# Kernel tuning notes

Hardware: AMD Instinct MI355X
Metric: run time of the kernel (lower is better)

## Reference

```python
import jax, jax.numpy as jnp
import numpy as np

D_IN = 1024
D_OUT = 1024
N_HEADS = 16
HEAD_DIM = D_OUT // N_HEADS


def setup_inputs() -> dict:
    key = jax.random.key(0)
    ks = jax.random.split(key, 5)
    scale = 0.02
    x = jax.random.normal(ks[0], (2, 2048, D_IN), dtype=jnp.float32)
    Wq = jax.random.normal(ks[1], (D_IN, D_OUT), dtype=jnp.float32) * scale
    Wk = jax.random.normal(ks[2], (D_IN, D_OUT), dtype=jnp.float32) * scale
    Wv = jax.random.normal(ks[3], (D_IN, D_OUT), dtype=jnp.float32) * scale
    Wout = jax.random.normal(ks[4], (D_OUT, D_OUT), dtype=jnp.float32) * scale
    return {"x": x, "Wq": Wq, "Wk": Wk, "Wv": Wv, "Wout": Wout}


def reference(x, Wq, Wk, Wv, Wout):
    batch, seq_len, _ = x.shape
    # projections (no bias)
    Q = (x @ Wq).reshape(batch, seq_len, N_HEADS, HEAD_DIM)
    K = (x @ Wk).reshape(batch, seq_len, N_HEADS, HEAD_DIM)
    V = (x @ Wv).reshape(batch, seq_len, N_HEADS, HEAD_DIM)
    # scores: [batch, heads, seq, seq]
    scores = jnp.einsum("bqhd,bkhd->bhqk", Q, K) / jnp.sqrt(
        jnp.asarray(HEAD_DIM, dtype=x.dtype)
    )
    # causal mask: positions k > q masked to -inf
    causal = jnp.tril(jnp.ones((seq_len, seq_len), dtype=bool))
    scores = jnp.where(causal[None, None], scores, -jnp.inf)
    weights = jax.nn.softmax(scores, axis=-1)
    vectors = jnp.einsum("bhqk,bkhd->bqhd", weights, V)
    vectors = vectors.reshape(batch, seq_len, D_OUT)
    return vectors @ Wout
```

## Files before the change

kernel.cpp:

```cpp
#include <hip/hip_runtime.h>
#include <hip/hip_bf16.h>


typedef __attribute__((ext_vector_type(8))) _Float16 vhalf8;
typedef __attribute__((ext_vector_type(4))) _Float16 vhalf4;
typedef __attribute__((ext_vector_type(4))) float vfloat4;

#define D_MODEL 1024
#define SEQ     2048
#define NB      2
#define NH      16
#define HD      64

#define SCALE_K1 0.18033688f

__device__ __forceinline__ void async16(const void* g, void* l) {
  __builtin_amdgcn_global_load_lds(
      (const __attribute__((address_space(1))) unsigned int*)g,
      (__attribute__((address_space(3))) unsigned int*)l, 16, 0, 0);
}

__global__ __launch_bounds__(256) void prep(
    const float* __restrict__ x,
    const float* __restrict__ Wq, const float* __restrict__ Wk,
    const float* __restrict__ Wv, const float* __restrict__ Wo,
    _Float16* __restrict__ Xh, _Float16* __restrict__ Wt_qkv,
    _Float16* __restrict__ Wot) {
  int z = blockIdx.z;
  int t = threadIdx.x;
  if (z == 4) {
    int id = blockIdx.y * 16 + blockIdx.x;
#pragma unroll
    for (int pass = 0; pass < 8; pass++) {
      size_t i = ((size_t)(pass * 256 + id) * 256 + t) * 8;
      float4 a = *(const float4*)&x[i];
      float4 b = *(const float4*)&x[i + 4];
      vhalf8 h;
      h[0] = (_Float16)a.x; h[1] = (_Float16)a.y;
      h[2] = (_Float16)a.z; h[3] = (_Float16)a.w;
      h[4] = (_Float16)b.x; h[5] = (_Float16)b.y;
      h[6] = (_Float16)b.z; h[7] = (_Float16)b.w;
      *(vhalf8*)&Xh[i] = h;
    }
    return;
  }
  __shared__ _Float16 tile[64][65];
  const float* in = (z == 0) ? Wq : (z == 1) ? Wk : (z == 2) ? Wv : Wo;
  _Float16* out = (z < 3) ? (Wt_qkv + (size_t)z * 1024 * 1024) : Wot;
  int c0 = blockIdx.x * 64, r0 = blockIdx.y * 64;
  int tc = t & 63, tr = t >> 6;
#pragma unroll
  for (int p = 0; p < 16; p++) {
    int r = tr + p * 4;
    tile[r][tc] = (_Float16)in[(size_t)(r0 + r) * 1024 + c0 + tc];
  }
  __syncthreads();
#pragma unroll
  for (int p = 0; p < 16; p++) {
    int r = tr + p * 4;
    out[(size_t)(c0 + r) * 1024 + r0 + tc] = tile[tc][r];
  }
}

template <int BN>
__global__ __launch_bounds__(256) void gemm128(
    const _Float16* __restrict__ A, const _Float16* __restrict__ Bt,
    _Float16* __restrict__ Ch, float* __restrict__ Cf,
    _Float16* __restrict__ Vt, int M, int N, int K, int mode) {
  constexpr int ACH = 8;
  constexpr int BCH = BN / 16;
  constexpr int CPW = (ACH + BCH) / 4;
  constexpr int JN = BN / 32;
  __shared__ _Float16 As[128 * 32];
  __shared__ _Float16 Bs[BN * 32];
  int m0 = blockIdx.x * 128, n0 = blockIdx.y * BN;
  int t = threadIdx.x;
  int lane = t & 63, wave = t >> 6;
  int wm = (wave >> 1) * 64, wn = (wave & 1) * (BN / 2);
  int col = lane & 15, quad = lane >> 4;
  int srow = lane >> 2;
  int gcol = (((lane & 3) ^ (srow & 3)) << 3);

  vfloat4 acc[4][JN];
#pragma unroll
  for (int i = 0; i < 4; i++)
#pragma unroll
    for (int j = 0; j < JN; j++) {
      acc[i][j][0] = 0.f; acc[i][j][1] = 0.f;
      acc[i][j][2] = 0.f; acc[i][j][3] = 0.f;
    }

  int xq = (quad ^ (col & 3)) * 8;

  for (int k0 = 0; k0 < K; k0 += 32) {
    __syncthreads();
#pragma unroll
    for (int j = 0; j < CPW; j++) {
      int c = wave * CPW + j;
      if (c < ACH) {
        int row = c * 16 + srow;
        async16(&A[(size_t)(m0 + row) * K + k0 + gcol], &As[c * 512]);
      } else {
        int row = (c - ACH) * 16 + srow;
        async16(&Bt[(size_t)(n0 + row) * K + k0 + gcol], &Bs[(c - ACH) * 512]);
      }
    }
    __syncthreads();

    vhalf8 af[4], bf[JN];
#pragma unroll
    for (int i = 0; i < 4; i++)
      af[i] = *(const vhalf8*)&As[(wm + i * 16 + col) * 32 + xq];
#pragma unroll
    for (int j = 0; j < JN; j++)
      bf[j] = *(const vhalf8*)&Bs[(wn + j * 16 + col) * 32 + xq];
#pragma unroll
    for (int i = 0; i < 4; i++)
#pragma unroll
      for (int j = 0; j < JN; j++)
        acc[i][j] = __builtin_amdgcn_mfma_f32_16x16x32_f16(af[i], bf[j], acc[i][j], 0, 0, 0);
  }

  bool vmode = (mode == 2) && (n0 >= 2048);
#pragma unroll
  for (int i = 0; i < 4; i++)
#pragma unroll
    for (int j = 0; j < JN; j++) {
      if (vmode) {
        int n = n0 + wn + j * 16 + col;
        int nn = n - 2048;
        int hh = nn >> 6, dd = nn & 63;
        int m_base = m0 + wm + i * 16 + quad * 4;
        int bb = m_base >> 11, ss = m_base & 2047;
        vhalf4 pk;
        pk[0] = (_Float16)acc[i][j][0]; pk[1] = (_Float16)acc[i][j][1];
        pk[2] = (_Float16)acc[i][j][2]; pk[3] = (_Float16)acc[i][j][3];
        *(vhalf4*)&Vt[(((size_t)bb * NH + hh) * HD + dd) * SEQ + ss] = pk;
      } else {
#pragma unroll
        for (int r = 0; r < 4; r++) {
          int m = m0 + wm + i * 16 + quad * 4 + r;
          int n = n0 + wn + j * 16 + col;
          if (mode == 1)
            Cf[(size_t)m * N + n] = acc[i][j][r];
          else
            Ch[(size_t)m * N + n] = (_Float16)acc[i][j][r];
        }
      }
    }
}

__global__ __launch_bounds__(256, 2) void attn(
    const _Float16* __restrict__ QKV, const _Float16* __restrict__ Vt,
    _Float16* __restrict__ Vec) {
  int blk = blockIdx.x;
  int pp = blk >> 5;
  int hb = blk & 31;
  int h = hb & 15;
  int b = hb >> 4;

  const _Float16* Qb  = QKV + (size_t)(b * SEQ) * 3072 + h * HD;
  const _Float16* Kb  = QKV + (size_t)(b * SEQ) * 3072 + 1024 + h * HD;
  const _Float16* Vtb = Vt + (size_t)(b * NH + h) * HD * SEQ;

  int t = threadIdx.x;
  int lane = t & 63, wave = t >> 6;
  int sw = wave & 1, hf = wave >> 1;
  int col = lane & 15, quad = lane >> 4;

  __shared__ union {
    _Float16 Ks[2][64][72];
    float    Om[64][65];
  } su;
  __shared__ _Float16 Vs[2][64][72];
  __shared__ _Float16 Ps[4][32][72];
  __shared__ float Lm[64];

  int tl = t & 127;
  int srow = tl >> 2;
  int scol = (tl & 3) * 16;
  int kslotA = ((srow & 3) << 4) + (srow >> 2);
  int kslotB = kslotA + 8;
  int kcol = scol ^ ((srow & 3) << 4);

  int tiles[2] = {31 - pp, pp};

  vhalf8 krA0, krA1, krB0, krB1, vrA0, vrA1, vrB0, vrB1;
  {
    const _Float16* kg = &Kb[(size_t)(hf * 64 + srow) * 3072 + scol];
    krA0 = *(const vhalf8*)kg; krA1 = *(const vhalf8*)(kg + 8);
    kg += (size_t)32 * 3072;
    krB0 = *(const vhalf8*)kg; krB1 = *(const vhalf8*)(kg + 8);
    const _Float16* vg = &Vtb[(size_t)srow * SEQ + hf * 64 + scol];
    vrA0 = *(const vhalf8*)vg; vrA1 = *(const vhalf8*)(vg + 8);
    vg += (size_t)32 * SEQ;
    vrB0 = *(const vhalf8*)vg; vrB1 = *(const vhalf8*)(vg + 8);
  }

#pragma unroll
  for (int phase = 0; phase < 2; phase++) {
    int qt = tiles[phase];
    int q0 = qt * 64;
    int ntk = qt + 1;
    int J = (ntk + 1) >> 1;
    int wq0 = q0 + sw * 32;

    vhalf8 qf0[2], qf1[2];
#pragma unroll
    for (int qs = 0; qs < 2; qs++) {
      const _Float16* qp = &Qb[(size_t)(wq0 + qs * 16 + col) * 3072 + quad * 8];
      qf0[qs] = *(const vhalf8*)qp;
      qf1[qs] = *(const vhalf8*)(qp + 32);
#pragma unroll
      for (int i = 0; i < 8; i++) {
        qf0[qs][i] = qf0[qs][i] * (_Float16)SCALE_K1;
        qf1[qs][i] = qf1[qs][i] * (_Float16)SCALE_K1;
      }
    }

    vfloat4 o[2][4];
#pragma unroll
    for (int qs = 0; qs < 2; qs++)
#pragma unroll
      for (int i = 0; i < 4; i++) {
        o[qs][i][0] = 0.f; o[qs][i][1] = 0.f;
        o[qs][i][2] = 0.f; o[qs][i][3] = 0.f;
      }
    float lsum[2][4] = {{0.f, 0.f, 0.f, 0.f}, {0.f, 0.f, 0.f, 0.f}};

    for (int j = 0; j < J; j++) {
      int ti = 2 * j + hf;
      bool active = (ti < ntk);
      int kb = ti * 64;
      if (active) {
        *(vhalf8*)&su.Ks[hf][kslotA][kcol]     = krA0;
        *(vhalf8*)&su.Ks[hf][kslotA][kcol + 8] = krA1;
        *(vhalf8*)&su.Ks[hf][kslotB][kcol]     = krB0;
        *(vhalf8*)&su.Ks[hf][kslotB][kcol + 8] = krB1;
        *(vhalf8*)&Vs[hf][srow][scol]          = vrA0;
        *(vhalf8*)&Vs[hf][srow][scol + 8]      = vrA1;
        *(vhalf8*)&Vs[hf][srow + 32][scol]     = vrB0;
        *(vhalf8*)&Vs[hf][srow + 32][scol + 8] = vrB1;
      }
      __syncthreads();

      {
        int tnext;
        if (phase == 0)
          tnext = (ti + 2 < ntk) ? (ti + 2) : hf;
        else
          tnext = (ti + 2 < ntk) ? (ti + 2) : ti;
        int kpf = tnext * 64;
        const _Float16* kg = &Kb[(size_t)(kpf + srow) * 3072 + scol];
        krA0 = *(const vhalf8*)kg; krA1 = *(const vhalf8*)(kg + 8);
        kg += (size_t)32 * 3072;
        krB0 = *(const vhalf8*)kg; krB1 = *(const vhalf8*)(kg + 8);
        const _Float16* vg = &Vtb[(size_t)srow * SEQ + kpf + scol];
        vrA0 = *(const vhalf8*)vg; vrA1 = *(const vhalf8*)(vg + 8);
        vg += (size_t)32 * SEQ;
        vrB0 = *(const vhalf8*)vg; vrB1 = *(const vhalf8*)(vg + 8);
      }

      if (active) {
        vhalf8 kf[4][2];
#pragma unroll
        for (int hh = 0; hh < 4; hh++) {
          int swz = hh << 4;
          kf[hh][0] = *(const vhalf8*)&su.Ks[hf][hh * 16 + col][(quad * 8) ^ swz];
          kf[hh][1] = *(const vhalf8*)&su.Ks[hf][hh * 16 + col][(32 + quad * 8) ^ swz];
        }
#pragma unroll
        for (int qs = 0; qs < 2; qs++) {
          int wq = wq0 + qs * 16;
          vfloat4 s[4];
#pragma unroll
          for (int hh = 0; hh < 4; hh++) {
            vfloat4 z; z[0]=0.f; z[1]=0.f; z[2]=0.f; z[3]=0.f;
            z = __builtin_amdgcn_mfma_f32_16x16x32_f16(qf0[qs], kf[hh][0], z, 0, 0, 0);
            z = __builtin_amdgcn_mfma_f32_16x16x32_f16(qf1[qs], kf[hh][1], z, 0, 0, 0);
            s[hh] = z;
          }
          bool diag = (kb + 63 > wq);
#pragma unroll
          for (int r = 0; r < 4; r++) {
            int q = wq + quad * 4 + r;
            float p[4];
#pragma unroll
            for (int hh = 0; hh < 4; hh++) {
              float sc = s[hh][r];
              if (diag && (kb + 4 * col + hh > q)) sc = -1e30f;
              p[hh] = __builtin_exp2f(sc);
            }
            lsum[qs][r] += (p[0] + p[1]) + (p[2] + p[3]);
            vhalf4 ph;
            ph[0] = (_Float16)p[0]; ph[1] = (_Float16)p[1];
            ph[2] = (_Float16)p[2]; ph[3] = (_Float16)p[3];
            *(vhalf4*)&Ps[wave][qs * 16 + quad * 4 + r][4 * col] = ph;
          }
        }
        __asm__ __volatile__("s_waitcnt lgkmcnt(0)" ::: "memory");
        vhalf8 pf0[2], pf1[2];
#pragma unroll
        for (int qs = 0; qs < 2; qs++) {
          pf0[qs] = *(const vhalf8*)&Ps[wave][qs * 16 + col][quad * 8];
          pf1[qs] = *(const vhalf8*)&Ps[wave][qs * 16 + col][32 + quad * 8];
        }
#pragma unroll
        for (int tt = 0; tt < 4; tt++) {
          vhalf8 vf0 = *(const vhalf8*)&Vs[hf][tt * 16 + col][quad * 8];
          vhalf8 vf1 = *(const vhalf8*)&Vs[hf][tt * 16 + col][32 + quad * 8];
#pragma unroll
          for (int qs = 0; qs < 2; qs++) {
            o[qs][tt] = __builtin_amdgcn_mfma_f32_16x16x32_f16(pf0[qs], vf0, o[qs][tt], 0, 0, 0);
            o[qs][tt] = __builtin_amdgcn_mfma_f32_16x16x32_f16(pf1[qs], vf1, o[qs][tt], 0, 0, 0);
          }
        }
      }
      __syncthreads();
    }

    float rs[2][4];
#pragma unroll
    for (int qs = 0; qs < 2; qs++)
#pragma unroll
      for (int r = 0; r < 4; r++) {
        float v = lsum[qs][r];
#pragma unroll
        for (int msk = 1; msk < 16; msk <<= 1) v += __shfl_xor(v, msk, 64);
        rs[qs][r] = v;
      }
    if (hf == 1) {
#pragma unroll
      for (int qs = 0; qs < 2; qs++) {
#pragma unroll
        for (int tt = 0; tt < 4; tt++)
#pragma unroll
          for (int r = 0; r < 4; r++)
            su.Om[sw * 32 + qs * 16 + quad * 4 + r][tt * 16 + col] = o[qs][tt][r];
        if (col == 0)
#pragma unroll
          for (int r = 0; r < 4; r++)
            Lm[sw * 32 + qs * 16 + quad * 4 + r] = rs[qs][r];
      }
    }
    __syncthreads();
    if (hf == 0) {
#pragma unroll
      for (int qs = 0; qs < 2; qs++) {
        float inv_l[4];
#pragma unroll
        for (int r = 0; r < 4; r++)
          inv_l[r] = 1.0f / (rs[qs][r] + Lm[sw * 32 + qs * 16 + quad * 4 + r]);
#pragma unroll
        for (int tt = 0; tt < 4; tt++)
#pragma unroll
          for (int r = 0; r < 4; r++) {
            int q = wq0 + qs * 16 + quad * 4 + r;
            int d = tt * 16 + col;
            float ov = o[qs][tt][r] +
                       su.Om[sw * 32 + qs * 16 + quad * 4 + r][tt * 16 + col];
            Vec[(size_t)(b * SEQ + q) * D_MODEL + h * HD + d] =
                (_Float16)(ov * inv_l[r]);
          }
      }
    }
    __syncthreads();
  }
}

extern "C" void kernel_launch(void* const* d_in, const int* in_sizes, int n_in,
                              void* d_out, int out_size, void* d_ws, size_t ws_size,
                              hipStream_t stream) {
  const float* x  = (const float*)d_in[0];
  const float* Wq = (const float*)d_in[1];
  const float* Wk = (const float*)d_in[2];
  const float* Wv = (const float*)d_in[3];
  const float* Wo = (const float*)d_in[4];
  float* out = (float*)d_out;

  char* ws = (char*)d_ws;
  _Float16* Xh     = (_Float16*)ws;
  _Float16* Wt_qkv = (_Float16*)(ws + 8388608);
  _Float16* Wot    = (_Float16*)(ws + 14680064);
  _Float16* QKV    = (_Float16*)(ws + 16777216);
  _Float16* Vt     = (_Float16*)(ws + 41943040);
  _Float16* Vec    = (_Float16*)(ws + 50331648);

  dim3 tb(256);
  prep<<<dim3(16, 16, 5), tb, 0, stream>>>(x, Wq, Wk, Wv, Wo, Xh, Wt_qkv, Wot);
  gemm128<128><<<dim3(32, 24), tb, 0, stream>>>(Xh, Wt_qkv, QKV, nullptr, Vt,
                                                4096, 3072, 1024, 2);
  attn<<<dim3(512), dim3(256), 0, stream>>>(QKV, Vt, Vec);
  gemm128<64><<<dim3(32, 16), tb, 0, stream>>>(Vec, Wot, nullptr, out, nullptr,
                                               4096, 1024, 1024, 1);
}
```

Before: 197.1 us.

## Enlarge attention blocks to 128 query rows with four-way key split

The attention kernel now launches 256 blocks of 1024 threads instead of 512 blocks of 256. Each block covers a 128-row query tile, paired causally as tiles 15-pp and pp, and spreads key tiles across four wave groups instead of two. Every K/V tile staged in LDS is now shared by twice as many query rows, which is meant to cut redundant global loads. In exchange the cross-group reduction of partial outputs and row sums goes through a larger LDS union in two stages, and LDS use of about 147KB allows only one block per CU. That gives roughly one wave of blocks across the GPU, and the higher launch-bound occupancy target may squeeze registers.

```diff
diff --git a/kernel.cpp b/kernel.cpp
--- a/kernel.cpp
+++ b/kernel.cpp
@@ -150,7 +150,7 @@
     }
 }
 
-__global__ __launch_bounds__(256, 2) void attn(
+__global__ __launch_bounds__(1024, 4) void attn(
     const _Float16* __restrict__ QKV, const _Float16* __restrict__ Vt,
     _Float16* __restrict__ Vec) {
   int blk = blockIdx.x;
@@ -165,44 +165,41 @@
 
   int t = threadIdx.x;
   int lane = t & 63, wave = t >> 6;
-  int sw = wave & 1, hf = wave >> 1;
+  int sw = wave & 3, hf = wave >> 2;
   int col = lane & 15, quad = lane >> 4;
 
+  __shared__ _Float16 Ks[4][64][72];
+  __shared__ _Float16 Vs[4][64][72];
   __shared__ union {
-    _Float16 Ks[2][64][72];
-    float    Om[64][65];
-  } su;
-  __shared__ _Float16 Vs[2][64][72];
-  __shared__ _Float16 Ps[4][32][72];
-  __shared__ float Lm[64];
-
-  int tl = t & 127;
+    _Float16 Ps[16][32][72];
+    struct {
+      float Om[2][128][66];
+      float Lm[4][128];
+    } m;
+  } pu;
+
+  int tl = t & 255;
   int srow = tl >> 2;
   int scol = (tl & 3) * 16;
-  int kslotA = ((srow & 3) << 4) + (srow >> 2);
-  int kslotB = kslotA + 8;
+  int kslot = ((srow & 3) << 4) + (srow >> 2);
   int kcol = scol ^ ((srow & 3) << 4);
 
-  int tiles[2] = {31 - pp, pp};
-
-  vhalf8 krA0, krA1, krB0, krB1, vrA0, vrA1, vrB0, vrB1;
+  int tiles[2] = {15 - pp, pp};
+
+  vhalf8 kr0, kr1, vr0, vr1;
   {
     const _Float16* kg = &Kb[(size_t)(hf * 64 + srow) * 3072 + scol];
-    krA0 = *(const vhalf8*)kg; krA1 = *(const vhalf8*)(kg + 8);
-    kg += (size_t)32 * 3072;
-    krB0 = *(const vhalf8*)kg; krB1 = *(const vhalf8*)(kg + 8);
+    kr0 = *(const vhalf8*)kg; kr1 = *(const vhalf8*)(kg + 8);
     const _Float16* vg = &Vtb[(size_t)srow * SEQ + hf * 64 + scol];
-    vrA0 = *(const vhalf8*)vg; vrA1 = *(const vhalf8*)(vg + 8);
-    vg += (size_t)32 * SEQ;
-    vrB0 = *(const vhalf8*)vg; vrB1 = *(const vhalf8*)(vg + 8);
+    vr0 = *(const vhalf8*)vg; vr1 = *(const vhalf8*)(vg + 8);
   }
 
 #pragma unroll
   for (int phase = 0; phase < 2; phase++) {
     int qt = tiles[phase];
-    int q0 = qt * 64;
-    int ntk = qt + 1;
-    int J = (ntk + 1) >> 1;
+    int q0 = qt * 128;
+    int ntk = 2 * qt + 2;
+    int J = (ntk + 3) >> 2;
     int wq0 = q0 + sw * 32;
 
     vhalf8 qf0[2], qf1[2];
@@ -229,36 +226,28 @@
     float lsum[2][4] = {{0.f, 0.f, 0.f, 0.f}, {0.f, 0.f, 0.f, 0.f}};
 
     for (int j = 0; j < J; j++) {
-      int ti = 2 * j + hf;
+      int ti = 4 * j + hf;
       bool active = (ti < ntk);
       int kb = ti * 64;
       if (active) {
-        *(vhalf8*)&su.Ks[hf][kslotA][kcol]     = krA0;
-        *(vhalf8*)&su.Ks[hf][kslotA][kcol + 8] = krA1;
-        *(vhalf8*)&su.Ks[hf][kslotB][kcol]     = krB0;
-        *(vhalf8*)&su.Ks[hf][kslotB][kcol + 8] = krB1;
-        *(vhalf8*)&Vs[hf][srow][scol]          = vrA0;
-        *(vhalf8*)&Vs[hf][srow][scol + 8]      = vrA1;
-        *(vhalf8*)&Vs[hf][srow + 32][scol]     = vrB0;
-        *(vhalf8*)&Vs[hf][srow + 32][scol + 8] = vrB1;
+        *(vhalf8*)&Ks[hf][kslot][kcol]     = kr0;
+        *(vhalf8*)&Ks[hf][kslot][kcol + 8] = kr1;
+        *(vhalf8*)&Vs[hf][srow][scol]      = vr0;
+        *(vhalf8*)&Vs[hf][srow][scol + 8]  = vr1;
       }
       __syncthreads();
 
       {
         int tnext;
         if (phase == 0)
-          tnext = (ti + 2 < ntk) ? (ti + 2) : hf;
+          tnext = (ti + 4 < ntk) ? (ti + 4) : hf;
         else
-          tnext = (ti + 2 < ntk) ? (ti + 2) : ti;
+          tnext = (ti + 4 < ntk) ? (ti + 4) : ti;
         int kpf = tnext * 64;
         const _Float16* kg = &Kb[(size_t)(kpf + srow) * 3072 + scol];
-        krA0 = *(const vhalf8*)kg; krA1 = *(const vhalf8*)(kg + 8);
-        kg += (size_t)32 * 3072;
-        krB0 = *(const vhalf8*)kg; krB1 = *(const vhalf8*)(kg + 8);
+        kr0 = *(const vhalf8*)kg; kr1 = *(const vhalf8*)(kg + 8);
         const _Float16* vg = &Vtb[(size_t)srow * SEQ + kpf + scol];
-        vrA0 = *(const vhalf8*)vg; vrA1 = *(const vhalf8*)(vg + 8);
-        vg += (size_t)32 * SEQ;
-        vrB0 = *(const vhalf8*)vg; vrB1 = *(const vhalf8*)(vg + 8);
+        vr0 = *(const vhalf8*)vg; vr1 = *(const vhalf8*)(vg + 8);
       }
 
       if (active) {
@@ -266,8 +255,8 @@
 #pragma unroll
         for (int hh = 0; hh < 4; hh++) {
           int swz = hh << 4;
-          kf[hh][0] = *(const vhalf8*)&su.Ks[hf][hh * 16 + col][(quad * 8) ^ swz];
-          kf[hh][1] = *(const vhalf8*)&su.Ks[hf][hh * 16 + col][(32 + quad * 8) ^ swz];
+          kf[hh][0] = *(const vhalf8*)&Ks[hf][hh * 16 + col][(quad * 8) ^ swz];
+          kf[hh][1] = *(const vhalf8*)&Ks[hf][hh * 16 + col][(32 + quad * 8) ^ swz];
         }
 #pragma unroll
         for (int qs = 0; qs < 2; qs++) {
@@ -295,15 +284,15 @@
             vhalf4 ph;
             ph[0] = (_Float16)p[0]; ph[1] = (_Float16)p[1];
             ph[2] = (_Float16)p[2]; ph[3] = (_Float16)p[3];
-            *(vhalf4*)&Ps[wave][qs * 16 + quad * 4 + r][4 * col] = ph;
+            *(vhalf4*)&pu.Ps[wave][qs * 16 + quad * 4 + r][4 * col] = ph;
           }
         }
         __asm__ __volatile__("s_waitcnt lgkmcnt(0)" ::: "memory");
         vhalf8 pf0[2], pf1[2];
 #pragma unroll
         for (int qs = 0; qs < 2; qs++) {
-          pf0[qs] = *(const vhalf8*)&Ps[wave][qs * 16 + col][quad * 8];
-          pf1[qs] = *(const vhalf8*)&Ps[wave][qs * 16 + col][32 + quad * 8];
+          pf0[qs] = *(const vhalf8*)&pu.Ps[wave][qs * 16 + col][quad * 8];
+          pf1[qs] = *(const vhalf8*)&pu.Ps[wave][qs * 16 + col][32 + quad * 8];
         }
 #pragma unroll
         for (int tt = 0; tt < 4; tt++) {
@@ -329,42 +318,74 @@
         for (int msk = 1; msk < 16; msk <<= 1) v += __shfl_xor(v, msk, 64);
         rs[qs][r] = v;
       }
-    if (hf == 1) {
-#pragma unroll
-      for (int qs = 0; qs < 2; qs++) {
+
+    if (hf == 1 || hf == 3) {
+      int pl = hf >> 1;
+#pragma unroll
+      for (int qs = 0; qs < 2; qs++)
 #pragma unroll
         for (int tt = 0; tt < 4; tt++)
 #pragma unroll
           for (int r = 0; r < 4; r++)
-            su.Om[sw * 32 + qs * 16 + quad * 4 + r][tt * 16 + col] = o[qs][tt][r];
-        if (col == 0)
+            pu.m.Om[pl][sw * 32 + qs * 16 + quad * 4 + r][tt * 16 + col] =
+                o[qs][tt][r];
+    }
+    if (hf != 0 && col == 0) {
+#pragma unroll
+      for (int qs = 0; qs < 2; qs++)
+#pragma unroll
+        for (int r = 0; r < 4; r++)
+          pu.m.Lm[hf][sw * 32 + qs * 16 + quad * 4 + r] = rs[qs][r];
+    }
+    __syncthreads();
+
+    if (hf == 2) {
+#pragma unroll
+      for (int qs = 0; qs < 2; qs++)
+#pragma unroll
+        for (int tt = 0; tt < 4; tt++)
+#pragma unroll
+          for (int r = 0; r < 4; r++) {
+            int rr = sw * 32 + qs * 16 + quad * 4 + r;
+            float v = o[qs][tt][r] + pu.m.Om[1][rr][tt * 16 + col];
+            pu.m.Om[1][rr][tt * 16 + col] = v;
+          }
+    }
+    if (hf == 0) {
+#pragma unroll
+      for (int qs = 0; qs < 2; qs++)
+#pragma unroll
+        for (int tt = 0; tt < 4; tt++)
 #pragma unroll
           for (int r = 0; r < 4; r++)
-            Lm[sw * 32 + qs * 16 + quad * 4 + r] = rs[qs][r];
-      }
+            o[qs][tt][r] += pu.m.Om[0][sw * 32 + qs * 16 + quad * 4 + r]
+                                    [tt * 16 + col];
     }
     __syncthreads();
+
     if (hf == 0) {
 #pragma unroll
       for (int qs = 0; qs < 2; qs++) {
         float inv_l[4];
 #pragma unroll
-        for (int r = 0; r < 4; r++)
-          inv_l[r] = 1.0f / (rs[qs][r] + Lm[sw * 32 + qs * 16 + quad * 4 + r]);
+        for (int r = 0; r < 4; r++) {
+          int rr = sw * 32 + qs * 16 + quad * 4 + r;
+          inv_l[r] = 1.0f / (rs[qs][r] + pu.m.Lm[1][rr] + pu.m.Lm[2][rr] +
+                             pu.m.Lm[3][rr]);
+        }
 #pragma unroll
         for (int tt = 0; tt < 4; tt++)
 #pragma unroll
           for (int r = 0; r < 4; r++) {
+            int rr = sw * 32 + qs * 16 + quad * 4 + r;
             int q = wq0 + qs * 16 + quad * 4 + r;
             int d = tt * 16 + col;
-            float ov = o[qs][tt][r] +
-                       su.Om[sw * 32 + qs * 16 + quad * 4 + r][tt * 16 + col];
+            float ov = o[qs][tt][r] + pu.m.Om[1][rr][tt * 16 + col];
             Vec[(size_t)(b * SEQ + q) * D_MODEL + h * HD + d] =
                 (_Float16)(ov * inv_l[r]);
           }
       }
     }
-    __syncthreads();
   }
 }
 
@@ -390,7 +411,7 @@
   prep<<<dim3(16, 16, 5), tb, 0, stream>>>(x, Wq, Wk, Wv, Wo, Xh, Wt_qkv, Wot);
   gemm128<128><<<dim3(32, 24), tb, 0, stream>>>(Xh, Wt_qkv, QKV, nullptr, Vt,
                                                 4096, 3072, 1024, 2);
-  attn<<<dim3(512), dim3(256), 0, stream>>>(QKV, Vt, Vec);
+  attn<<<dim3(256), dim3(1024), 0, stream>>>(QKV, Vt, Vec);
   gemm128<64><<<dim3(32, 16), tb, 0, stream>>>(Vec, Wot, nullptr, out, nullptr,
                                                4096, 1024, 1024, 1);
 }
```

Result: slower. 247.7 us (+25.7%).
